# Kernel tuning notes

Hardware: AMD Instinct MI355X
Metric: run time of the kernel (lower is better)

## Reference

```python
import jax, jax.numpy as jnp
import numpy as np

D_MODEL = 1024
NUM_HEADS = 16
GROUPS = 4
HEADS_PER_GROUP = NUM_HEADS // GROUPS
D_K = D_MODEL // NUM_HEADS
B, S = 2, 2048


def setup_inputs() -> dict:
    key = jax.random.key(0)
    ks = jax.random.split(key, 10)
    sc = 0.02
    return {
        "x": jax.random.normal(ks[0], (B, S, D_MODEL), dtype=jnp.float32),
        "W_Q": jax.random.normal(ks[1], (D_MODEL, D_MODEL), dtype=jnp.float32) * sc,
        "b_Q": jnp.zeros((D_MODEL,), dtype=jnp.float32),
        "W_K": jax.random.normal(ks[2], (GROUPS, D_MODEL, D_K), dtype=jnp.float32) * sc,
        "b_K": jnp.zeros((GROUPS, D_K), dtype=jnp.float32),
        "W_V": jax.random.normal(ks[3], (GROUPS, D_MODEL, D_K), dtype=jnp.float32) * sc,
        "b_V": jnp.zeros((GROUPS, D_K), dtype=jnp.float32),
        "W_O": jax.random.normal(ks[4], (D_MODEL, D_MODEL), dtype=jnp.float32) * sc,
        "b_O": jnp.zeros((D_MODEL,), dtype=jnp.float32),
    }


def reference(x, W_Q, b_Q, W_K, b_K, W_V, b_V, W_O, b_O):
    b, s, _ = x.shape
    # Q: [b, s, d_model] -> [b, groups, heads_per_group, s, d_k]
    Q = (x @ W_Q + b_Q).reshape(b, s, NUM_HEADS, D_K).transpose(0, 2, 1, 3)
    Q = Q.reshape(b, GROUPS, HEADS_PER_GROUP, s, D_K)
    # Shared K/V per group: [b, groups, s, d_k]
    K = jnp.einsum('bsd,gdk->bgsk', x, W_K) + b_K[None, :, None, :]
    V = jnp.einsum('bsd,gdk->bgsk', x, W_V) + b_V[None, :, None, :]
    # scores: [b, groups, heads_per_group, s, s]
    scores = jnp.einsum('bghsk,bgtk->bghst', Q, K) / jnp.sqrt(jnp.float32(D_K))
    attn = jax.nn.softmax(scores, axis=-1)
    # context: [b, groups, heads_per_group, s, d_k] -> [b, s, d_model]
    ctx = jnp.einsum('bghst,bgtk->bghsk', attn, V)
    ctx = ctx.reshape(b, NUM_HEADS, s, D_K).transpose(0, 2, 1, 3).reshape(b, s, D_MODEL)
    return ctx @ W_O + b_O
```

## Files before the change

### kernel.cpp

```cpp
#include <hip/hip_runtime.h>
#include <cstdint>
#include <cstddef>

typedef short bf16x8 __attribute__((ext_vector_type(8)));
typedef float f32x4 __attribute__((ext_vector_type(4)));

#define DM 1024
#define NHEADS 16
#define NGROUPS 4
#define DK 64
#define BATCH 2
#define SEQ 2048
#define MROWS 4096

#define QB_ELEMS   ((size_t)BATCH*NHEADS*SEQ*DK)
#define KB_ELEMS   ((size_t)BATCH*NGROUPS*SEQ*DK)
#define VT_ELEMS   KB_ELEMS
#define XC_ELEMS   ((size_t)MROWS*DM)
#define WQKV_ELEMS ((size_t)1536*DM)
#define WO_ELEMS   ((size_t)DM*DM)

#define SCL_Q 0.180336880f

__device__ __forceinline__ ushort f2bf(float f) {
    union { float f; uint32_t u; } a; a.f = f;
    uint32_t u = a.u;
    return (ushort)((u + 0x7FFFu + ((u >> 16) & 1u)) >> 16);
}

__device__ __forceinline__ void gll16(const void* g, void* l) {
    __builtin_amdgcn_global_load_lds((const __attribute__((address_space(1))) void*)g,
                                     (__attribute__((address_space(3))) void*)l, 16, 0, 0);
}

__device__ __forceinline__ void transpose_tile(
        const float* __restrict__ src, int src_ld, ushort* __restrict__ dst,
        int r0, int c0, int tid, float (*tl)[65])
{
    const int rr = tid >> 4, cc = (tid & 15) * 4;
#pragma unroll
    for (int p = 0; p < 4; p++) {
        int r = rr + p * 16;
        float4 v = *(const float4*)(src + (size_t)(r0 + r) * src_ld + c0 + cc);
        tl[cc + 0][r] = v.x; tl[cc + 1][r] = v.y;
        tl[cc + 2][r] = v.z; tl[cc + 3][r] = v.w;
    }
    __syncthreads();
#pragma unroll
    for (int p = 0; p < 4; p++) {
        int c = rr + p * 16;
        ushort4 o;
        o.x = f2bf(tl[c][cc + 0]); o.y = f2bf(tl[c][cc + 1]);
        o.z = f2bf(tl[c][cc + 2]); o.w = f2bf(tl[c][cc + 3]);
        *(ushort4*)(dst + (size_t)(c0 + c) * 1024 + r0 + cc) = o;
    }
}

__global__ __launch_bounds__(256) void gqa_prep_kernel(
        const float* __restrict__ x,
        const float* __restrict__ WQ, const float* __restrict__ WK,
        const float* __restrict__ WV,
        const float* __restrict__ bQ, const float* __restrict__ bK,
        const float* __restrict__ bV,
        ushort* __restrict__ xbf, ushort* __restrict__ WqkvT,
        float* __restrict__ bcat)
{
    __shared__ float tl[64][65];
    const int bid = blockIdx.x, tid = threadIdx.x;
    if (bid < 256) {
        transpose_tile(WQ, 1024, WqkvT, (bid >> 4) * 64, (bid & 15) * 64, tid, tl);
    } else if (bid < 320) {
        int t = bid - 256, g = t >> 4;
        transpose_tile(WK + (size_t)g * 1024 * 64, 64,
                       WqkvT + (size_t)(1024 + g * 64) * 1024,
                       (t & 15) * 64, 0, tid, tl);
    } else if (bid < 384) {
        int t = bid - 320, g = t >> 4;
        transpose_tile(WV + (size_t)g * 1024 * 64, 64,
                       WqkvT + (size_t)(1280 + g * 64) * 1024,
                       (t & 15) * 64, 0, tid, tl);
    } else if (bid < 640) {
        int cid = bid - 384;
        const float* xs = x + (size_t)cid * 16384;
        ushort* xd = xbf + (size_t)cid * 16384;
#pragma unroll
        for (int p = 0; p < 16; p++) {
            float4 v = *(const float4*)(xs + p * 1024 + tid * 4);
            ushort4 o = { f2bf(v.x), f2bf(v.y), f2bf(v.z), f2bf(v.w) };
            *(ushort4*)(xd + p * 1024 + tid * 4) = o;
        }
    } else {
        for (int i = tid; i < 1536; i += 256) {
            float v = (i < 1024) ? bQ[i] : (i < 1280 ? bK[i - 1024] : bV[i - 1280]);
            bcat[i] = v;
        }
    }
}

template<bool QKV_EPI, int BN, bool RIDERS>
__global__ __launch_bounds__(256, 4) void gqa_gemm_kernel(
        const ushort* __restrict__ A, const ushort* __restrict__ BT,
        const float* __restrict__ bias, float* __restrict__ outF,
        ushort* __restrict__ Qb, ushort* __restrict__ Kb, ushort* __restrict__ Vtg,
        const float* __restrict__ WO, ushort* __restrict__ WoT)
{
    __shared__ ushort smem[4][4096];
    const int tid = threadIdx.x;
    int i = blockIdx.x;

    if constexpr (RIDERS) {
        if (i < 256) {
            float (*tl)[65] = (float(*)[65])&smem[0][0];
            transpose_tile(WO, 1024, WoT, (i >> 4) * 64, (i & 15) * 64, tid, tl);
            return;
        }
        i -= 256;
    }

    const int xcd = i & 7, slot = i >> 3;
    const int bm = (slot / BN) * 8 + xcd;
    const int bn = slot % BN;
    const int wave = tid >> 6, lane = tid & 63;
    const int wm = (wave & 1) * 32, wn = (wave >> 1) * 32;
    const int lr = lane & 15, lq = lane >> 4;
    const int swz = lr & 7;

    const ushort* srcA[2]; const ushort* srcB[2]; int dstOff[2];
#pragma unroll
    for (int p = 0; p < 2; p++) {
        int slt = p * 256 + tid;
        int row = slt >> 3, cb = (slt & 7) ^ (row & 7);
        srcA[p] = A  + (size_t)(bm * 64 + row) * 1024 + cb * 8;
        srcB[p] = BT + (size_t)(bn * 64 + row) * 1024 + cb * 8;
        dstOff[p] = p * 2048 + wave * 512;
    }

    f32x4 acc[2][2];
#pragma unroll
    for (int ii = 0; ii < 2; ii++)
#pragma unroll
        for (int j = 0; j < 2; j++) acc[ii][j] = (f32x4){0.f, 0.f, 0.f, 0.f};

#pragma unroll
    for (int p = 0; p < 2; p++) {
        gll16(srcA[p], &smem[0][dstOff[p]]);
        gll16(srcB[p], &smem[2][dstOff[p]]);
    }

    for (int kt = 0; kt < 16; kt++) {
        __syncthreads();
        if (kt < 15) {
            int buf = (kt + 1) & 1, ko = (kt + 1) * 64;
#pragma unroll
            for (int p = 0; p < 2; p++) {
                gll16(srcA[p] + ko, &smem[buf][dstOff[p]]);
                gll16(srcB[p] + ko, &smem[2 + buf][dstOff[p]]);
            }
        }
        const ushort* as = smem[kt & 1];
        const ushort* bs = smem[2 + (kt & 1)];
        bf16x8 af[2][2], bfr[2][2];
#pragma unroll
        for (int kh = 0; kh < 2; kh++) {
#pragma unroll
            for (int ii = 0; ii < 2; ii++)
                af[kh][ii] = *(const bf16x8*)&as[(wm + ii * 16 + lr) * 64 + ((kh * 4 + lq) ^ swz) * 8];
#pragma unroll
            for (int j = 0; j < 2; j++)
                bfr[kh][j] = *(const bf16x8*)&bs[(wn + j * 16 + lr) * 64 + ((kh * 4 + lq) ^ swz) * 8];
        }
#pragma unroll
        for (int kh = 0; kh < 2; kh++)
#pragma unroll
            for (int ii = 0; ii < 2; ii++)
#pragma unroll
                for (int j = 0; j < 2; j++)
                    acc[ii][j] = __builtin_amdgcn_mfma_f32_16x16x32_bf16(af[kh][ii], bfr[kh][j], acc[ii][j], 0, 0, 0);
    }

#pragma unroll
    for (int ii = 0; ii < 2; ii++) {
        int mg = bm * 64 + wm + ii * 16 + lq * 4;
        int b = mg >> 11, s = mg & 2047;
#pragma unroll
        for (int j = 0; j < 2; j++) {
            int cg = bn * 64 + wn + j * 16 + lr;
            float bv = bias[cg];
            if constexpr (QKV_EPI) {
                int d = cg & 63;
                if (cg < 1024) {
                    int h = cg >> 6;
                    ushort* dst = Qb + ((size_t)(b * NHEADS + h) * SEQ + s) * DK + d;
#pragma unroll
                    for (int r = 0; r < 4; r++)
                        dst[r * DK] = f2bf((acc[ii][j][r] + bv) * SCL_Q);
                } else if (cg < 1280) {
                    int g = (cg - 1024) >> 6;
                    ushort* dst = Kb + ((size_t)(b * NGROUPS + g) * SEQ + s) * DK + d;
#pragma unroll
                    for (int r = 0; r < 4; r++) dst[r * DK] = f2bf(acc[ii][j][r] + bv);
                } else {
                    int g = (cg - 1280) >> 6;
                    int s4 = s >> 2, kg = s4 & 7;
                    int col = ((s4 >> 3) << 5) + (((((kg & 3) << 1) | (kg >> 2))) << 2);
                    ushort4 pk;
                    pk.x = f2bf(acc[ii][j][0] + bv); pk.y = f2bf(acc[ii][j][1] + bv);
                    pk.z = f2bf(acc[ii][j][2] + bv); pk.w = f2bf(acc[ii][j][3] + bv);
                    *(ushort4*)(Vtg + ((size_t)(b * NGROUPS + g) * DK + d) * SEQ + col) = pk;
                }
            } else {
#pragma unroll
                for (int r = 0; r < 4; r++)
                    outF[(size_t)(mg + r) * DM + cg] = acc[ii][j][r] + bv;
            }
        }
    }
}

__global__ __launch_bounds__(256, 2) void gqa_attn_kernel(
        const ushort* __restrict__ Qb, const ushort* __restrict__ Kb,
        const ushort* __restrict__ Vtg, ushort* __restrict__ ctx)
{
    __shared__ ushort smem[2][2][64 * 64];
    __shared__ float accX[2][4][16];

    const int tid = threadIdx.x, wave = tid >> 6, lane = tid & 63;
    const int lr = lane & 15, lq = lane >> 4;
    const int swz = lr & 7;
    const int wq = wave & 1, wt = wave >> 1;
    const int i = blockIdx.x;
    const int bg = i & 7, s2 = i >> 3;
    const int qt = s2 & 15, h = s2 >> 4;
    const int b = bg >> 2, g = bg & 3, hg = g * 4 + h;

    const ushort* Qh = Qb  + (size_t)(b * NHEADS  + hg) * SEQ * DK;
    const ushort* Kg = Kb  + (size_t)(b * NGROUPS + g)  * SEQ * DK;
    const ushort* Vg = Vtg + (size_t)(b * NGROUPS + g)  * DK * SEQ;

    const int s0 = qt * 128 + wq * 64;
    const int tb = wt * 32;

    bf16x8 qf[4][2];
#pragma unroll
    for (int qs = 0; qs < 4; qs++)
#pragma unroll
        for (int kh = 0; kh < 2; kh++)
            qf[qs][kh] = *(const bf16x8*)(Qh + (size_t)(s0 + qs * 16 + lr) * DK + kh * 32 + lq * 8);

    const ushort* srcK[2]; const ushort* srcV[2]; int dstOff[2];
#pragma unroll
    for (int p = 0; p < 2; p++) {
        int slt = p * 256 + tid;
        int row = slt >> 3, cb = (slt & 7) ^ (row & 7);
        srcK[p] = Kg + (size_t)row * DK + cb * 8;
        srcV[p] = Vg + (size_t)row * SEQ + cb * 8;
        dstOff[p] = p * 2048 + wave * 512;
    }

    f32x4 of[4][4];
#pragma unroll
    for (int qs = 0; qs < 4; qs++)
#pragma unroll
        for (int j = 0; j < 4; j++) of[qs][j] = (f32x4){0.f, 0.f, 0.f, 0.f};
    f32x4 accL[4];
#pragma unroll
    for (int qs = 0; qs < 4; qs++) accL[qs] = (f32x4){0.f, 0.f, 0.f, 0.f};

    bf16x8 ones;
#pragma unroll
    for (int k = 0; k < 8; k++) ones[k] = (short)0x3F80;

#pragma unroll
    for (int p = 0; p < 2; p++) {
        gll16(srcK[p], &smem[0][0][dstOff[p]]);
        gll16(srcV[p], &smem[1][0][dstOff[p]]);
    }

    for (int it = 0; it < 32; it++) {
        __syncthreads();
        if (it < 31) {
            int buf = (it + 1) & 1, t0 = (it + 1) * 64;
#pragma unroll
            for (int p = 0; p < 2; p++) {
                gll16(srcK[p] + (size_t)t0 * DK, &smem[0][buf][dstOff[p]]);
                gll16(srcV[p] + t0, &smem[1][buf][dstOff[p]]);
            }
        }
        const ushort* ks = smem[0][it & 1];
        const ushort* vs = smem[1][it & 1];

        bf16x8 kf[2][2];
#pragma unroll
        for (int nt = 0; nt < 2; nt++)
#pragma unroll
            for (int kh = 0; kh < 2; kh++)
                kf[nt][kh] = *(const bf16x8*)&ks[((tb + nt * 16 + lr) * 8 + ((kh * 4 + lq) ^ swz)) * 8];

        bf16x8 vf[4];
#pragma unroll
        for (int j = 0; j < 4; j++)
            vf[j] = *(const bf16x8*)&vs[((j * 16 + lr) * 8 + ((wt * 4 + lq) ^ swz)) * 8];

        f32x4 sc[4][2];
#pragma unroll
        for (int qs = 0; qs < 4; qs++)
#pragma unroll
            for (int nt = 0; nt < 2; nt++) {
                f32x4 s = (f32x4){0.f, 0.f, 0.f, 0.f};
                s = __builtin_amdgcn_mfma_f32_16x16x32_bf16(kf[nt][0], qf[qs][0], s, 0, 0, 0);
                s = __builtin_amdgcn_mfma_f32_16x16x32_bf16(kf[nt][1], qf[qs][1], s, 0, 0, 0);
                sc[qs][nt] = s;
            }

        union PF { bf16x8 v; uint32_t w[4]; };
        PF pf[4];
#pragma unroll
        for (int qs = 0; qs < 4; qs++) {
#pragma unroll
            for (int nt = 0; nt < 2; nt++) {
                union { float f; uint32_t u; } e0, e1, e2, e3;
                e0.f = __builtin_amdgcn_exp2f(sc[qs][nt][0]);
                e1.f = __builtin_amdgcn_exp2f(sc[qs][nt][1]);
                e2.f = __builtin_amdgcn_exp2f(sc[qs][nt][2]);
                e3.f = __builtin_amdgcn_exp2f(sc[qs][nt][3]);
                pf[qs].w[nt * 2 + 0] = __builtin_amdgcn_perm(e1.u, e0.u, 0x07060302u);
                pf[qs].w[nt * 2 + 1] = __builtin_amdgcn_perm(e3.u, e2.u, 0x07060302u);
            }
            accL[qs] = __builtin_amdgcn_mfma_f32_16x16x32_bf16(ones, pf[qs].v, accL[qs], 0, 0, 0);
        }

#pragma unroll
        for (int qs = 0; qs < 4; qs++)
#pragma unroll
            for (int j = 0; j < 4; j++)
                of[qs][j] = __builtin_amdgcn_mfma_f32_16x16x32_bf16(vf[j], pf[qs].v, of[qs][j], 0, 0, 0);
    }

    __syncthreads();
    float* comb = (float*)&smem[0][0][0];
    if (wt == 1) {
        float* cw = comb + wq * 4096;
#pragma unroll
        for (int qs = 0; qs < 4; qs++)
#pragma unroll
            for (int j = 0; j < 4; j++)
                *(f32x4*)&cw[(qs * 4 + j) * 256 + lane * 4] = of[qs][j];
        if (lq == 0) {
#pragma unroll
            for (int qs = 0; qs < 4; qs++) accX[wq][qs][lr] = accL[qs][0];
        }
    }
    __syncthreads();
    if (wt == 0) {
        const float* cw = comb + wq * 4096;
        float inv[4];
#pragma unroll
        for (int qs = 0; qs < 4; qs++)
            inv[qs] = 1.0f / (accL[qs][0] + accX[wq][qs][lr]);
        ushort* cbp = ctx + (size_t)b * SEQ * DM;
#pragma unroll
        for (int qs = 0; qs < 4; qs++) {
            int s = s0 + qs * 16 + lr;
#pragma unroll
            for (int j = 0; j < 4; j++) {
                f32x4 o2 = of[qs][j] + *(const f32x4*)&cw[(qs * 4 + j) * 256 + lane * 4];
                ushort4 o;
                o.x = f2bf(o2[0] * inv[qs]);
                o.y = f2bf(o2[1] * inv[qs]);
                o.z = f2bf(o2[2] * inv[qs]);
                o.w = f2bf(o2[3] * inv[qs]);
                *(ushort4*)(cbp + (size_t)s * DM + hg * 64 + j * 16 + lq * 4) = o;
            }
        }
    }
}

extern "C" void kernel_launch(void* const* d_in, const int* in_sizes, int n_in,
                              void* d_out, int out_size, void* d_ws, size_t ws_size,
                              hipStream_t stream) {
    const float* x  = (const float*)d_in[0];
    const float* WQ = (const float*)d_in[1];
    const float* bQ = (const float*)d_in[2];
    const float* WK = (const float*)d_in[3];
    const float* bK = (const float*)d_in[4];
    const float* WV = (const float*)d_in[5];
    const float* bV = (const float*)d_in[6];
    const float* WO = (const float*)d_in[7];
    const float* bO = (const float*)d_in[8];

    ushort* Qb    = (ushort*)d_ws;
    ushort* Kb    = Qb + QB_ELEMS;
    ushort* Vtg   = Kb + KB_ELEMS;
    ushort* xc    = Vtg + VT_ELEMS;
    ushort* WqkvT = xc + XC_ELEMS;
    ushort* WoT   = WqkvT + WQKV_ELEMS;
    float*  bcat  = (float*)(WoT + WO_ELEMS);

    gqa_prep_kernel<<<641, 256, 0, stream>>>(x, WQ, WK, WV, bQ, bK, bV,
                                             xc, WqkvT, bcat);
    gqa_gemm_kernel<true, 24, true><<<1792, 256, 0, stream>>>(
        xc, WqkvT, bcat, nullptr, Qb, Kb, Vtg, WO, WoT);
    gqa_attn_kernel<<<512, 256, 0, stream>>>(Qb, Kb, Vtg, xc);
    gqa_gemm_kernel<false, 16, false><<<1024, 256, 0, stream>>>(
        xc, WoT, bO, (float*)d_out, nullptr, nullptr, nullptr, nullptr, nullptr);
}
```

Measured before the change: 160.7 us.

## Drop LDS staging; load GEMM and attention operands directly from global into registers

Both the projection GEMMs and the attention kernel stop staging tiles through shared memory with global_load_lds and barriers. Each wave now owns its own 64x64 output tile (GEMM) or its own 64-query head slice (attention) and streams operands from global memory into registers, double-buffered. Attention also replaces the ones-vector MFMA row-sum with scalar accumulation plus shuffles, and the cross-wave LDS reduction is removed. Grid sizes shrink to match. This removes barrier and LDS overhead, at the cost of redundant global/L2 traffic, since tiles are no longer shared across waves, and lower occupancy.

```diff
diff --git a/kernel.cpp b/kernel.cpp
--- a/kernel.cpp
+++ b/kernel.cpp
@@ -26,11 +26,6 @@
     union { float f; uint32_t u; } a; a.f = f;
     uint32_t u = a.u;
     return (ushort)((u + 0x7FFFu + ((u >> 16) & 1u)) >> 16);
-}
-
-__device__ __forceinline__ void gll16(const void* g, void* l) {
-    __builtin_amdgcn_global_load_lds((const __attribute__((address_space(1))) void*)g,
-                                     (__attribute__((address_space(3))) void*)l, 16, 0, 0);
 }
 
 __device__ __forceinline__ void transpose_tile(
@@ -97,94 +92,81 @@
     }
 }
 
-template<bool QKV_EPI, int BN, bool RIDERS>
-__global__ __launch_bounds__(256, 4) void gqa_gemm_kernel(
+template<bool QKV_EPI>
+__global__ __launch_bounds__(256, 2) void gqa_gemm_kernel(
         const ushort* __restrict__ A, const ushort* __restrict__ BT,
         const float* __restrict__ bias, float* __restrict__ outF,
         ushort* __restrict__ Qb, ushort* __restrict__ Kb, ushort* __restrict__ Vtg,
         const float* __restrict__ WO, ushort* __restrict__ WoT)
 {
-    __shared__ ushort smem[4][4096];
     const int tid = threadIdx.x;
-    int i = blockIdx.x;
-
-    if constexpr (RIDERS) {
-        if (i < 256) {
-            float (*tl)[65] = (float(*)[65])&smem[0][0];
-            transpose_tile(WO, 1024, WoT, (i >> 4) * 64, (i & 15) * 64, tid, tl);
+    int blk = blockIdx.x;
+
+    if constexpr (QKV_EPI) {
+        if (blk < 256) {
+            __shared__ float tl[64][65];
+            transpose_tile(WO, 1024, WoT, (blk >> 4) * 64, (blk & 15) * 64, tid, tl);
             return;
         }
-        i -= 256;
-    }
-
-    const int xcd = i & 7, slot = i >> 3;
-    const int bm = (slot / BN) * 8 + xcd;
-    const int bn = slot % BN;
+        blk -= 256;
+    }
+
     const int wave = tid >> 6, lane = tid & 63;
-    const int wm = (wave & 1) * 32, wn = (wave >> 1) * 32;
     const int lr = lane & 15, lq = lane >> 4;
-    const int swz = lr & 7;
-
-    const ushort* srcA[2]; const ushort* srcB[2]; int dstOff[2];
-#pragma unroll
-    for (int p = 0; p < 2; p++) {
-        int slt = p * 256 + tid;
-        int row = slt >> 3, cb = (slt & 7) ^ (row & 7);
-        srcA[p] = A  + (size_t)(bm * 64 + row) * 1024 + cb * 8;
-        srcB[p] = BT + (size_t)(bn * 64 + row) * 1024 + cb * 8;
-        dstOff[p] = p * 2048 + wave * 512;
-    }
-
-    f32x4 acc[2][2];
-#pragma unroll
-    for (int ii = 0; ii < 2; ii++)
-#pragma unroll
-        for (int j = 0; j < 2; j++) acc[ii][j] = (f32x4){0.f, 0.f, 0.f, 0.f};
-
-#pragma unroll
-    for (int p = 0; p < 2; p++) {
-        gll16(srcA[p], &smem[0][dstOff[p]]);
-        gll16(srcB[p], &smem[2][dstOff[p]]);
-    }
-
-    for (int kt = 0; kt < 16; kt++) {
-        __syncthreads();
-        if (kt < 15) {
-            int buf = (kt + 1) & 1, ko = (kt + 1) * 64;
-#pragma unroll
-            for (int p = 0; p < 2; p++) {
-                gll16(srcA[p] + ko, &smem[buf][dstOff[p]]);
-                gll16(srcB[p] + ko, &smem[2 + buf][dstOff[p]]);
-            }
-        }
-        const ushort* as = smem[kt & 1];
-        const ushort* bs = smem[2 + (kt & 1)];
-        bf16x8 af[2][2], bfr[2][2];
-#pragma unroll
-        for (int kh = 0; kh < 2; kh++) {
-#pragma unroll
-            for (int ii = 0; ii < 2; ii++)
-                af[kh][ii] = *(const bf16x8*)&as[(wm + ii * 16 + lr) * 64 + ((kh * 4 + lq) ^ swz) * 8];
-#pragma unroll
-            for (int j = 0; j < 2; j++)
-                bfr[kh][j] = *(const bf16x8*)&bs[(wn + j * 16 + lr) * 64 + ((kh * 4 + lq) ^ swz) * 8];
-        }
-#pragma unroll
-        for (int kh = 0; kh < 2; kh++)
-#pragma unroll
-            for (int ii = 0; ii < 2; ii++)
-#pragma unroll
-                for (int j = 0; j < 2; j++)
-                    acc[ii][j] = __builtin_amdgcn_mfma_f32_16x16x32_bf16(af[kh][ii], bfr[kh][j], acc[ii][j], 0, 0, 0);
-    }
-
-#pragma unroll
-    for (int ii = 0; ii < 2; ii++) {
-        int mg = bm * 64 + wm + ii * 16 + lq * 4;
+    const int xcd = blk & 7, sb = blk >> 3;
+    const int bm = xcd * 8 + (sb & 7);
+    const int bn = (sb >> 3) * 4 + wave;
+
+    const ushort* aRow[4]; const ushort* bRow[4];
+#pragma unroll
+    for (int i = 0; i < 4; i++)
+        aRow[i] = A  + (size_t)(bm * 64 + i * 16 + lr) * 1024 + lq * 8;
+#pragma unroll
+    for (int j = 0; j < 4; j++)
+        bRow[j] = BT + (size_t)(bn * 64 + j * 16 + lr) * 1024 + lq * 8;
+
+    f32x4 acc[4][4];
+#pragma unroll
+    for (int i = 0; i < 4; i++)
+#pragma unroll
+        for (int j = 0; j < 4; j++) acc[i][j] = (f32x4){0.f, 0.f, 0.f, 0.f};
+
+    bf16x8 a0[4], b0[4], a1[4], b1[4];
+#pragma unroll
+    for (int i = 0; i < 4; i++) a0[i] = *(const bf16x8*)(aRow[i]);
+#pragma unroll
+    for (int j = 0; j < 4; j++) b0[j] = *(const bf16x8*)(bRow[j]);
+
+    for (int kt = 0; kt < 32; kt += 2) {
+#pragma unroll
+        for (int i = 0; i < 4; i++) a1[i] = *(const bf16x8*)(aRow[i] + (kt + 1) * 32);
+#pragma unroll
+        for (int j = 0; j < 4; j++) b1[j] = *(const bf16x8*)(bRow[j] + (kt + 1) * 32);
+#pragma unroll
+        for (int i = 0; i < 4; i++)
+#pragma unroll
+            for (int j = 0; j < 4; j++)
+                acc[i][j] = __builtin_amdgcn_mfma_f32_16x16x32_bf16(a0[i], b0[j], acc[i][j], 0, 0, 0);
+        if (kt + 2 < 32) {
+#pragma unroll
+            for (int i = 0; i < 4; i++) a0[i] = *(const bf16x8*)(aRow[i] + (kt + 2) * 32);
+#pragma unroll
+            for (int j = 0; j < 4; j++) b0[j] = *(const bf16x8*)(bRow[j] + (kt + 2) * 32);
+        }
+#pragma unroll
+        for (int i = 0; i < 4; i++)
+#pragma unroll
+            for (int j = 0; j < 4; j++)
+                acc[i][j] = __builtin_amdgcn_mfma_f32_16x16x32_bf16(a1[i], b1[j], acc[i][j], 0, 0, 0);
+    }
+
+#pragma unroll
+    for (int i = 0; i < 4; i++) {
+        int mg = bm * 64 + i * 16 + lq * 4;
         int b = mg >> 11, s = mg & 2047;
 #pragma unroll
-        for (int j = 0; j < 2; j++) {
-            int cg = bn * 64 + wn + j * 16 + lr;
+        for (int j = 0; j < 4; j++) {
+            int cg = bn * 64 + j * 16 + lr;
             float bv = bias[cg];
             if constexpr (QKV_EPI) {
                 int d = cg & 63;
@@ -193,25 +175,25 @@
                     ushort* dst = Qb + ((size_t)(b * NHEADS + h) * SEQ + s) * DK + d;
 #pragma unroll
                     for (int r = 0; r < 4; r++)
-                        dst[r * DK] = f2bf((acc[ii][j][r] + bv) * SCL_Q);
+                        dst[r * DK] = f2bf((acc[i][j][r] + bv) * SCL_Q);
                 } else if (cg < 1280) {
                     int g = (cg - 1024) >> 6;
                     ushort* dst = Kb + ((size_t)(b * NGROUPS + g) * SEQ + s) * DK + d;
 #pragma unroll
-                    for (int r = 0; r < 4; r++) dst[r * DK] = f2bf(acc[ii][j][r] + bv);
+                    for (int r = 0; r < 4; r++) dst[r * DK] = f2bf(acc[i][j][r] + bv);
                 } else {
                     int g = (cg - 1280) >> 6;
                     int s4 = s >> 2, kg = s4 & 7;
                     int col = ((s4 >> 3) << 5) + (((((kg & 3) << 1) | (kg >> 2))) << 2);
                     ushort4 pk;
-                    pk.x = f2bf(acc[ii][j][0] + bv); pk.y = f2bf(acc[ii][j][1] + bv);
-                    pk.z = f2bf(acc[ii][j][2] + bv); pk.w = f2bf(acc[ii][j][3] + bv);
+                    pk.x = f2bf(acc[i][j][0] + bv); pk.y = f2bf(acc[i][j][1] + bv);
+                    pk.z = f2bf(acc[i][j][2] + bv); pk.w = f2bf(acc[i][j][3] + bv);
                     *(ushort4*)(Vtg + ((size_t)(b * NGROUPS + g) * DK + d) * SEQ + col) = pk;
                 }
             } else {
 #pragma unroll
                 for (int r = 0; r < 4; r++)
-                    outF[(size_t)(mg + r) * DM + cg] = acc[ii][j][r] + bv;
+                    outF[(size_t)(mg + r) * DM + cg] = acc[i][j][r] + bv;
             }
         }
     }
@@ -221,25 +203,20 @@
         const ushort* __restrict__ Qb, const ushort* __restrict__ Kb,
         const ushort* __restrict__ Vtg, ushort* __restrict__ ctx)
 {
-    __shared__ ushort smem[2][2][64 * 64];
-    __shared__ float accX[2][4][16];
-
     const int tid = threadIdx.x, wave = tid >> 6, lane = tid & 63;
     const int lr = lane & 15, lq = lane >> 4;
-    const int swz = lr & 7;
-    const int wq = wave & 1, wt = wave >> 1;
-    const int i = blockIdx.x;
-    const int bg = i & 7, s2 = i >> 3;
-    const int qt = s2 & 15, h = s2 >> 4;
-    const int b = bg >> 2, g = bg & 3, hg = g * 4 + h;
+    const int blk = blockIdx.x;
+    const int bg = blk & 7;
+    const int r = (blk >> 3) * 4 + wave;
+    const int b = bg >> 2, g = bg & 3;
+    const int h = r & 3, qt = r >> 2;
+    const int hg = g * 4 + h;
+    const int s0 = qt * 64;
 
     const ushort* Qh = Qb  + (size_t)(b * NHEADS  + hg) * SEQ * DK;
     const ushort* Kg = Kb  + (size_t)(b * NGROUPS + g)  * SEQ * DK;
     const ushort* Vg = Vtg + (size_t)(b * NGROUPS + g)  * DK * SEQ;
 
-    const int s0 = qt * 128 + wq * 64;
-    const int tb = wt * 32;
-
     bf16x8 qf[4][2];
 #pragma unroll
     for (int qs = 0; qs < 4; qs++)
@@ -247,60 +224,39 @@
         for (int kh = 0; kh < 2; kh++)
             qf[qs][kh] = *(const bf16x8*)(Qh + (size_t)(s0 + qs * 16 + lr) * DK + kh * 32 + lq * 8);
 
-    const ushort* srcK[2]; const ushort* srcV[2]; int dstOff[2];
-#pragma unroll
-    for (int p = 0; p < 2; p++) {
-        int slt = p * 256 + tid;
-        int row = slt >> 3, cb = (slt & 7) ^ (row & 7);
-        srcK[p] = Kg + (size_t)row * DK + cb * 8;
-        srcV[p] = Vg + (size_t)row * SEQ + cb * 8;
-        dstOff[p] = p * 2048 + wave * 512;
-    }
+    const ushort* kB[2][2]; const ushort* vB[4];
+#pragma unroll
+    for (int nt = 0; nt < 2; nt++)
+#pragma unroll
+        for (int kh = 0; kh < 2; kh++)
+            kB[nt][kh] = Kg + (size_t)(nt * 16 + lr) * DK + (kh * 4 + lq) * 8;
+#pragma unroll
+    for (int j = 0; j < 4; j++)
+        vB[j] = Vg + (size_t)(j * 16 + lr) * SEQ + lq * 8;
 
     f32x4 of[4][4];
 #pragma unroll
     for (int qs = 0; qs < 4; qs++)
 #pragma unroll
         for (int j = 0; j < 4; j++) of[qs][j] = (f32x4){0.f, 0.f, 0.f, 0.f};
-    f32x4 accL[4];
-#pragma unroll
-    for (int qs = 0; qs < 4; qs++) accL[qs] = (f32x4){0.f, 0.f, 0.f, 0.f};
-
-    bf16x8 ones;
-#pragma unroll
-    for (int k = 0; k < 8; k++) ones[k] = (short)0x3F80;
-
-#pragma unroll
-    for (int p = 0; p < 2; p++) {
-        gll16(srcK[p], &smem[0][0][dstOff[p]]);
-        gll16(srcV[p], &smem[1][0][dstOff[p]]);
-    }
-
-    for (int it = 0; it < 32; it++) {
-        __syncthreads();
-        if (it < 31) {
-            int buf = (it + 1) & 1, t0 = (it + 1) * 64;
-#pragma unroll
-            for (int p = 0; p < 2; p++) {
-                gll16(srcK[p] + (size_t)t0 * DK, &smem[0][buf][dstOff[p]]);
-                gll16(srcV[p] + t0, &smem[1][buf][dstOff[p]]);
-            }
-        }
-        const ushort* ks = smem[0][it & 1];
-        const ushort* vs = smem[1][it & 1];
-
-        bf16x8 kf[2][2];
+    float lsum[4] = {0.f, 0.f, 0.f, 0.f};
+
+    bf16x8 kf0[2][2], vf0[4], kf1[2][2], vf1[4];
+
+    auto ldkv = [&](bf16x8 kf[2][2], bf16x8 vf[4], int it) {
+        const int ko = it * 32 * DK;
+        const int vo = it * 32;
 #pragma unroll
         for (int nt = 0; nt < 2; nt++)
 #pragma unroll
             for (int kh = 0; kh < 2; kh++)
-                kf[nt][kh] = *(const bf16x8*)&ks[((tb + nt * 16 + lr) * 8 + ((kh * 4 + lq) ^ swz)) * 8];
-
-        bf16x8 vf[4];
+                kf[nt][kh] = *(const bf16x8*)(kB[nt][kh] + ko);
 #pragma unroll
         for (int j = 0; j < 4; j++)
-            vf[j] = *(const bf16x8*)&vs[((j * 16 + lr) * 8 + ((wt * 4 + lq) ^ swz)) * 8];
-
+            vf[j] = *(const bf16x8*)(vB[j] + vo);
+    };
+
+    auto step = [&](bf16x8 kf[2][2], bf16x8 vf[4]) {
         f32x4 sc[4][2];
 #pragma unroll
         for (int qs = 0; qs < 4; qs++)
@@ -311,7 +267,6 @@
                 s = __builtin_amdgcn_mfma_f32_16x16x32_bf16(kf[nt][1], qf[qs][1], s, 0, 0, 0);
                 sc[qs][nt] = s;
             }
-
         union PF { bf16x8 v; uint32_t w[4]; };
         PF pf[4];
 #pragma unroll
@@ -323,54 +278,46 @@
                 e1.f = __builtin_amdgcn_exp2f(sc[qs][nt][1]);
                 e2.f = __builtin_amdgcn_exp2f(sc[qs][nt][2]);
                 e3.f = __builtin_amdgcn_exp2f(sc[qs][nt][3]);
+                lsum[qs] += (e0.f + e1.f) + (e2.f + e3.f);
                 pf[qs].w[nt * 2 + 0] = __builtin_amdgcn_perm(e1.u, e0.u, 0x07060302u);
                 pf[qs].w[nt * 2 + 1] = __builtin_amdgcn_perm(e3.u, e2.u, 0x07060302u);
             }
-            accL[qs] = __builtin_amdgcn_mfma_f32_16x16x32_bf16(ones, pf[qs].v, accL[qs], 0, 0, 0);
-        }
-
+        }
 #pragma unroll
         for (int qs = 0; qs < 4; qs++)
 #pragma unroll
             for (int j = 0; j < 4; j++)
                 of[qs][j] = __builtin_amdgcn_mfma_f32_16x16x32_bf16(vf[j], pf[qs].v, of[qs][j], 0, 0, 0);
-    }
-
-    __syncthreads();
-    float* comb = (float*)&smem[0][0][0];
-    if (wt == 1) {
-        float* cw = comb + wq * 4096;
-#pragma unroll
-        for (int qs = 0; qs < 4; qs++)
-#pragma unroll
-            for (int j = 0; j < 4; j++)
-                *(f32x4*)&cw[(qs * 4 + j) * 256 + lane * 4] = of[qs][j];
-        if (lq == 0) {
-#pragma unroll
-            for (int qs = 0; qs < 4; qs++) accX[wq][qs][lr] = accL[qs][0];
-        }
-    }
-    __syncthreads();
-    if (wt == 0) {
-        const float* cw = comb + wq * 4096;
-        float inv[4];
-#pragma unroll
-        for (int qs = 0; qs < 4; qs++)
-            inv[qs] = 1.0f / (accL[qs][0] + accX[wq][qs][lr]);
-        ushort* cbp = ctx + (size_t)b * SEQ * DM;
-#pragma unroll
-        for (int qs = 0; qs < 4; qs++) {
-            int s = s0 + qs * 16 + lr;
-#pragma unroll
-            for (int j = 0; j < 4; j++) {
-                f32x4 o2 = of[qs][j] + *(const f32x4*)&cw[(qs * 4 + j) * 256 + lane * 4];
-                ushort4 o;
-                o.x = f2bf(o2[0] * inv[qs]);
-                o.y = f2bf(o2[1] * inv[qs]);
-                o.z = f2bf(o2[2] * inv[qs]);
-                o.w = f2bf(o2[3] * inv[qs]);
-                *(ushort4*)(cbp + (size_t)s * DM + hg * 64 + j * 16 + lq * 4) = o;
-            }
+    };
+
+    ldkv(kf0, vf0, 0);
+    for (int it = 0; it < 64; it += 2) {
+        ldkv(kf1, vf1, it + 1);
+        step(kf0, vf0);
+        if (it + 2 < 64) ldkv(kf0, vf0, it + 2);
+        step(kf1, vf1);
+    }
+
+    float inv[4];
+#pragma unroll
+    for (int qs = 0; qs < 4; qs++) {
+        float v = lsum[qs];
+        v += __shfl_xor(v, 16);
+        v += __shfl_xor(v, 32);
+        inv[qs] = 1.0f / v;
+    }
+    ushort* cbp = ctx + (size_t)b * SEQ * DM;
+#pragma unroll
+    for (int qs = 0; qs < 4; qs++) {
+        int s = s0 + qs * 16 + lr;
+#pragma unroll
+        for (int j = 0; j < 4; j++) {
+            ushort4 o;
+            o.x = f2bf(of[qs][j][0] * inv[qs]);
+            o.y = f2bf(of[qs][j][1] * inv[qs]);
+            o.z = f2bf(of[qs][j][2] * inv[qs]);
+            o.w = f2bf(of[qs][j][3] * inv[qs]);
+            *(ushort4*)(cbp + (size_t)s * DM + hg * 64 + j * 16 + lq * 4) = o;
         }
     }
 }
@@ -398,9 +345,9 @@
 
     gqa_prep_kernel<<<641, 256, 0, stream>>>(x, WQ, WK, WV, bQ, bK, bV,
                                              xc, WqkvT, bcat);
-    gqa_gemm_kernel<true, 24, true><<<1792, 256, 0, stream>>>(
+    gqa_gemm_kernel<true><<<640, 256, 0, stream>>>(
         xc, WqkvT, bcat, nullptr, Qb, Kb, Vtg, WO, WoT);
-    gqa_attn_kernel<<<512, 256, 0, stream>>>(Qb, Kb, Vtg, xc);
-    gqa_gemm_kernel<false, 16, false><<<1024, 256, 0, stream>>>(
+    gqa_attn_kernel<<<256, 256, 0, stream>>>(Qb, Kb, Vtg, xc);
+    gqa_gemm_kernel<false><<<256, 256, 0, stream>>>(
         xc, WoT, bO, (float*)d_out, nullptr, nullptr, nullptr, nullptr, nullptr);
 }
```

Result: slower. 267.4 us (+66.4%).
